# Kernel tuning notes

Measured on AMD Instinct MI355X. Metric: run time of the kernel, lower is better.

Reference implementation:

```python
import jax, jax.numpy as jnp
import numpy as np

N, E = 50000, 800000
IN, HID, OUT = 128, 32, 8


def setup_inputs() -> dict:
    key = jax.random.key(0)
    ks = jax.random.split(key, 20)
    f32 = jnp.float32
    def rn(k, shape, s=0.1):
        return (jax.random.normal(k, shape, dtype=f32) * s)
    return {
        'x': jax.random.normal(ks[0], (N, IN), dtype=f32),
        'edge_index': jax.random.randint(ks[1], (2, E), 0, N, dtype=jnp.int32),
        'edge_attr': jax.random.uniform(ks[2], (E, 1), dtype=f32),
        # layer 1: heads=4, out=HID, concat -> 4*HID channels
        'w1l': rn(ks[3], (IN, 4 * HID)), 'b1l': rn(ks[4], (4 * HID,)),
        'w1r': rn(ks[5], (IN, 4 * HID)), 'b1r': rn(ks[6], (4 * HID,)),
        'w1e': rn(ks[7], (1, 4 * HID)),
        'att1': rn(ks[8], (4, HID)), 'bias1': rn(ks[9], (4 * HID,)),
        # layer 2: heads=2, out=HID, mean over heads -> HID channels
        'w2l': rn(ks[10], (4 * HID, 2 * HID)), 'b2l': rn(ks[11], (2 * HID,)),
        'w2r': rn(ks[12], (4 * HID, 2 * HID)), 'b2r': rn(ks[13], (2 * HID,)),
        'w2e': rn(ks[14], (1, 2 * HID)),
        'att2': rn(ks[15], (2, HID)), 'bias2': rn(ks[16], (HID,)),
        'wc': rn(ks[17], (HID, OUT)), 'bc': rn(ks[18], (OUT,)),
    }


def _add_self_loops(edge_index, edge_attr, n):
    # PyG GATv2Conv adds self-loops; edge feature for loops = mean of edge_attr
    loop = jnp.arange(n, dtype=edge_index.dtype)
    src = jnp.concatenate([edge_index[0], loop])
    dst = jnp.concatenate([edge_index[1], loop])
    mean_attr = jnp.broadcast_to(edge_attr.mean(axis=0), (n, edge_attr.shape[1]))
    ea = jnp.concatenate([edge_attr, mean_attr], axis=0)
    return src, dst, ea


def _gatv2(x, src, dst, eattr, Wl, bl, Wr, br, We, att, bias, heads, out, concat):
    n = x.shape[0]
    xl = (x @ Wl + bl).reshape(n, heads, out)   # source transform (messages)
    xr = (x @ Wr + br).reshape(n, heads, out)   # target transform
    e = (eattr @ We).reshape(-1, heads, out)    # edge embedding
    z = jax.nn.leaky_relu(xl[src] + xr[dst] + e, negative_slope=0.2)  # [Etot,H,D]
    score = jnp.einsum('ehd,hd->eh', z, att)
    # segment softmax over incoming edges of each destination node
    smax = jax.ops.segment_max(score, dst, num_segments=n)
    ex = jnp.exp(score - smax[dst])
    denom = jax.ops.segment_sum(ex, dst, num_segments=n)
    alpha = ex / denom[dst]                     # [Etot,H]
    agg = jax.ops.segment_sum(xl[src] * alpha[..., None], dst, num_segments=n)
    o = agg.reshape(n, heads * out) if concat else agg.mean(axis=1)
    return o + bias


def reference(x, edge_index, edge_attr, w1l, b1l, w1r, b1r, w1e, att1, bias1,
              w2l, b2l, w2r, b2r, w2e, att2, bias2, wc, bc):
    src, dst, ea = _add_self_loops(edge_index, edge_attr, x.shape[0])
    h = _gatv2(x, src, dst, ea, w1l, b1l, w1r, b1r, w1e, att1, bias1, 4, HID, True)
    h = jax.nn.elu(h)
    # dropout p=0.4 is training-only; reference is eval mode (identity)
    h = _gatv2(h, src, dst, ea, w2l, b2l, w2r, b2r, w2e, att2, bias2, 2, HID, False)
    h = jax.nn.elu(h)
    return h @ wc + bc
```

## Files before the change

kernel.cpp:

```cpp
#include <hip/hip_runtime.h>
#include <hip/hip_fp16.h>
#include <math.h>

typedef _Float16 h2_t __attribute__((ext_vector_type(2)));
typedef _Float16 h4_t __attribute__((ext_vector_type(4)));
typedef _Float16 h8_t __attribute__((ext_vector_type(8)));
typedef float f4_t __attribute__((ext_vector_type(4)));
typedef float f8_t __attribute__((ext_vector_type(8)));

#define PRE_BLOCKS 512
#define SB 512
#define NBUK_PAD 800

__device__ inline h8_t load8f_to_h8(const float* p) {
    float4 a = *(const float4*)p;
    float4 b = *(const float4*)(p + 4);
    h8_t r;
    r[0] = (_Float16)a.x; r[1] = (_Float16)a.y; r[2] = (_Float16)a.z; r[3] = (_Float16)a.w;
    r[4] = (_Float16)b.x; r[5] = (_Float16)b.y; r[6] = (_Float16)b.z; r[7] = (_Float16)b.w;
    return r;
}

__device__ inline h4_t load4f_to_h4(const float* p) {
    float4 a = *(const float4*)p;
    h4_t r;
    r[0] = (_Float16)a.x; r[1] = (_Float16)a.y; r[2] = (_Float16)a.z; r[3] = (_Float16)a.w;
    return r;
}

__device__ inline float dot8h(h8_t a, h8_t b, float s) {
    s = __builtin_amdgcn_fdot2(__builtin_shufflevector(a, a, 0, 1),
                               __builtin_shufflevector(b, b, 0, 1), s, false);
    s = __builtin_amdgcn_fdot2(__builtin_shufflevector(a, a, 2, 3),
                               __builtin_shufflevector(b, b, 2, 3), s, false);
    s = __builtin_amdgcn_fdot2(__builtin_shufflevector(a, a, 4, 5),
                               __builtin_shufflevector(b, b, 4, 5), s, false);
    s = __builtin_amdgcn_fdot2(__builtin_shufflevector(a, a, 6, 7),
                               __builtin_shufflevector(b, b, 6, 7), s, false);
    return s;
}

__device__ inline float dot4h(h4_t a, h4_t b, float s) {
    s = __builtin_amdgcn_fdot2(__builtin_shufflevector(a, a, 0, 1),
                               __builtin_shufflevector(b, b, 0, 1), s, false);
    s = __builtin_amdgcn_fdot2(__builtin_shufflevector(a, a, 2, 3),
                               __builtin_shufflevector(b, b, 2, 3), s, false);
    return s;
}

__device__ inline float elu1(float v) { return v > 0.f ? v : __expf(v) - 1.f; }

struct MA {
    const float* x;
    const float* eattr;
    const int* ei;
    const float *w1l, *b1l, *w1r, *b1r, *w1e, *att1, *bias1;
    const float *w2l, *b2l, *w2r, *b2r, *w2e, *att2, *bias2;
    const float *wc, *bc;
    float* out;
    _Float16 *xh, *xl1h, *xr1h, *h1h, *xl2h, *xr2h;
    _Float16 *p1l, *p1r, *p2l, *p2r;
    int *deg, *offb;
    unsigned* parth;
    unsigned *tstart, *tot;
    unsigned* smeanq;
    unsigned long long* tmp;
    unsigned* flags;
    float* part;
    unsigned* edges;
    int N, E, NW, NBK, CE;
    float invE;
};


__device__ inline void phase_packw(const MA& a, int g) {
    const float* W;
    _Float16* P;
    int M, lg;
    if (g < 2048)      { W = a.w1l; P = a.p1l; M = 128; lg = g; }
    else if (g < 4096) { W = a.w1r; P = a.p1r; M = 128; lg = g - 2048; }
    else if (g < 5120) { W = a.w2l; P = a.p2l; M = 64;  lg = g - 4096; }
    else               { W = a.w2r; P = a.p2r; M = 64;  lg = g - 5120; }
    int ln = lg & 63;
    int s = (lg >> 6) & 3;
    int tt = lg >> 8;
    int m = ln & 15, quad = ln >> 4;
    h8_t v;
#pragma unroll
    for (int j = 0; j < 8; ++j)
        v[j] = (_Float16)W[(size_t)(s * 32 + quad * 8 + j) * M + tt * 16 + m];
    *(h8_t*)(P + (size_t)lg * 8) = v;
}

template <int NT>
__device__ inline void phase_mm_tile(const MA& a, const _Float16* X, int rt, int lane,
                                     const _Float16* Pl, const float* bl, _Float16* Yl,
                                     const _Float16* Pr, const float* br, _Float16* Yr) {
    int nrow = lane & 15, quad = lane >> 4;
    int row = rt * 16 + nrow;
    if (row >= a.N) return;
    const _Float16* xp = X + (size_t)row * 128 + quad * 8;
    h8_t bf0 = *(const h8_t*)(xp);
    h8_t bf1 = *(const h8_t*)(xp + 32);
    h8_t bf2 = *(const h8_t*)(xp + 64);
    h8_t bf3 = *(const h8_t*)(xp + 96);
#pragma unroll
    for (int w = 0; w < 2; ++w) {
        const _Float16* P = w ? Pr : Pl;
        const float* bias = w ? br : bl;
        _Float16* Y = w ? Yr : Yl;
#pragma unroll
        for (int t2 = 0; t2 < NT; ++t2) {
            f4_t acc = {0.f, 0.f, 0.f, 0.f};
            const _Float16* pb = P + (size_t)t2 * 2048 + (size_t)lane * 8;
            acc = __builtin_amdgcn_mfma_f32_16x16x32_f16(*(const h8_t*)pb, bf0, acc, 0, 0, 0);
            acc = __builtin_amdgcn_mfma_f32_16x16x32_f16(*(const h8_t*)(pb + 512), bf1, acc, 0, 0, 0);
            acc = __builtin_amdgcn_mfma_f32_16x16x32_f16(*(const h8_t*)(pb + 1024), bf2, acc, 0, 0, 0);
            acc = __builtin_amdgcn_mfma_f32_16x16x32_f16(*(const h8_t*)(pb + 1536), bf3, acc, 0, 0, 0);
            float4 bv = *(const float4*)(bias + t2 * 16 + quad * 4);
            h4_t o;
            o[0] = (_Float16)(acc[0] + bv.x);
            o[1] = (_Float16)(acc[1] + bv.y);
            o[2] = (_Float16)(acc[2] + bv.z);
            o[3] = (_Float16)(acc[3] + bv.w);
            *(h4_t*)(Y + (size_t)row * (NT * 16) + t2 * 16 + quad * 4) = o;
        }
    }
}


__global__ __launch_bounds__(256) void k_pre(MA a) {
    if (blockIdx.x >= PRE_BLOCKS) {
        int g = (blockIdx.x - PRE_BLOCKS) * 256 + threadIdx.x;
        if (g < 6144) phase_packw(a, g);
        return;
    }
    __shared__ unsigned bh[NBUK_PAD];
    __shared__ float sd[4];
    int tx = threadIdx.x;
    for (int j = tx; j < NBUK_PAD; j += 256) bh[j] = 0u;

    int t = blockIdx.x * 256 + tx;
    const int stride = PRE_BLOCKS * 256;
    for (int i = t; i < NBUK_PAD; i += stride) a.flags[i] = 0u;
    int nchunk = (a.N * 128) >> 3;
    for (int i = t; i < nchunk; i += stride) {
        h8_t v = load8f_to_h8(a.x + (size_t)i * 8);
        *(h8_t*)(a.xh + (size_t)i * 8) = v;
    }
    float s = 0.f;
    for (int i = t; i < a.E; i += stride) s += a.eattr[i];
    for (int o = 1; o < 64; o <<= 1) s += __shfl_xor(s, o, 64);
    if ((tx & 63) == 0) sd[tx >> 6] = s;
    __syncthreads();
    if (tx == 0) a.part[blockIdx.x] = sd[0] + sd[1] + sd[2] + sd[3];

    int e0 = blockIdx.x * a.CE, e1 = min(e0 + a.CE, a.E);
    for (int e = e0 + tx; e < e1; e += 256)
        atomicAdd(&bh[((unsigned)a.ei[a.E + e]) >> 6], 1u);
    __syncthreads();
    for (int j = tx; j < NBUK_PAD; j += 256)
        a.parth[(size_t)blockIdx.x * NBUK_PAD + j] = bh[j];
}


__global__ __launch_bounds__(512, 1) void k_colscan(MA a) {
    __shared__ unsigned lds[512];
    __shared__ unsigned sbase;
    __shared__ float sd[8];
    int tx = threadIdx.x;
    int b = blockIdx.x;
    unsigned v = a.parth[(size_t)tx * NBUK_PAD + b];
    lds[tx] = v;
    __syncthreads();
    for (int o = 1; o < 512; o <<= 1) {
        unsigned u = (tx >= o) ? lds[tx - o] : 0u;
        __syncthreads();
        lds[tx] += u;
        __syncthreads();
    }
    unsigned T = lds[511];
    unsigned excl = lds[tx] - v;
    if (tx == 0) {
        unsigned run = 0;
        if (b == 0) {
            atomicExch(&a.flags[0], (2u << 30) | T);
        } else {
            atomicExch(&a.flags[b], (1u << 30) | T);
            int j = b - 1;
            while (true) {
                unsigned f = atomicAdd(&a.flags[j], 0u);
                unsigned st = f >> 30;
                if (st == 0u) continue;
                run += f & 0x3FFFFFFFu;
                if (st == 2u) break;
                --j;
            }
            atomicExch(&a.flags[b], (2u << 30) | (run + T));
        }
        a.tstart[b] = run;
        a.tot[b] = T;
        sbase = run;
    }
    __syncthreads();
    a.parth[(size_t)tx * NBUK_PAD + b] = sbase + excl;

    if (b == 0) {
        float s = a.part[tx];
        for (int o = 1; o < 64; o <<= 1) s += __shfl_xor(s, o, 64);
        if ((tx & 63) == 0) sd[tx >> 6] = s;
        __syncthreads();
        if (tx == 0) {
            float m = 0.f;
#pragma unroll
            for (int k = 0; k < 8; ++k) m += sd[k];
            a.smeanq[0] = (unsigned)__float2int_rn(m * a.invE * 255.f);
        }
    }
}


__global__ __launch_bounds__(256) void k_scatter(MA a) {
    int bid = blockIdx.x;
    if (bid < a.NW) {
        int wid = bid * 4 + (threadIdx.x >> 6);
        int ntile = (a.N + 15) / 16;
        if (wid < ntile)
            phase_mm_tile<8>(a, a.xh, wid, threadIdx.x & 63,
                             a.p1l, a.b1l, a.xl1h, a.p1r, a.b1r, a.xr1h);
        return;
    }
    __shared__ unsigned cur[NBUK_PAD];
    int s = bid - a.NW;
    int tx = threadIdx.x;
    for (int j = tx; j < NBUK_PAD; j += 256)
        cur[j] = a.parth[(size_t)s * NBUK_PAD + j];
    __syncthreads();
    int e0 = s * a.CE, e1 = min(e0 + a.CE, a.E);
    for (int e = e0 + tx; e < e1; e += 256) {
        int d = a.ei[a.E + e];
        unsigned src = (unsigned)a.ei[e];
        unsigned q = (unsigned)__float2int_rn(a.eattr[e] * 255.f);
        unsigned pos = atomicAdd(&cur[d >> 6], 1u);
        a.tmp[pos] = ((unsigned long long)(unsigned)(d & 63) << 32) |
                     (unsigned long long)(src | (q << 24));
    }
}


__global__ __launch_bounds__(256) void k_fine(MA a) {
    __shared__ int hist[64];
    __shared__ unsigned cur[64];
    __shared__ unsigned sm;
    int b = blockIdx.x;
    int tx = threadIdx.x;
    int n0 = b << 6;
    int nn = min(64, a.N - n0);
    unsigned ts = a.tstart[b], T = a.tot[b];
    if (tx < 64) hist[tx] = 0;
    if (tx == 0) sm = a.smeanq[0];
    __syncthreads();
    for (unsigned i = tx; i < T; i += 256) {
        unsigned long long v = a.tmp[ts + i];
        atomicAdd(&hist[(int)((v >> 32) & 63)], 1);
    }
    __syncthreads();
    if (tx < 64) {
        int deg1 = hist[tx] + 1;
        int vsc = deg1;
#pragma unroll
        for (int o = 1; o < 64; o <<= 1) {
            int u = __shfl_up(vsc, o, 64);
            if (tx >= o) vsc += u;
        }
        int off = (int)ts + n0 + (vsc - deg1);
        if (tx < nn) {
            a.offb[n0 + tx] = off;
            a.deg[n0 + tx] = deg1;
            a.edges[off] = (unsigned)(n0 + tx) | (sm << 24);
        }
        cur[tx] = (unsigned)(off + 1);
    }
    __syncthreads();
    for (unsigned i = tx; i < T; i += 256) {
        unsigned long long v = a.tmp[ts + i];
        int loc = (int)((v >> 32) & 63);
        unsigned pos = atomicAdd(&cur[loc], 1u);
        a.edges[pos] = (unsigned)v;
    }
}


__global__ __launch_bounds__(256) void k_node1(MA a) {
    int lane = threadIdx.x & 63;
    int node = blockIdx.x * 4 + (threadIdx.x >> 6);
    if (node >= a.N) return;
    int g = lane >> 4;
    int q = lane & 15;
    int c0 = q * 8;

    h8_t xrv = *(const h8_t*)(a.xr1h + (size_t)node * 128 + c0);
    h8_t wev = load8f_to_h8(a.w1e + c0);
    h8_t atv = load8f_to_h8(a.att1 + c0);
    int start = a.offb[node];
    int deg1 = a.deg[node];
    int last = deg1 - 1;

    float l = 0.f;
    f8_t acc = {0.f, 0.f, 0.f, 0.f, 0.f, 0.f, 0.f, 0.f};
    for (int i = 0; i < deg1; i += 16) {
        int s0 = i + g, s1 = i + 4 + g, s2 = i + 8 + g, s3 = i + 12 + g;
        unsigned p0 = a.edges[start + min(s0, last)];
        unsigned p1 = a.edges[start + min(s1, last)];
        unsigned p2 = a.edges[start + min(s2, last)];
        unsigned p3 = a.edges[start + min(s3, last)];
        h8_t x0 = *(const h8_t*)(a.xl1h + (size_t)(p0 & 0x00FFFFFFu) * 128 + c0);
        h8_t x1 = *(const h8_t*)(a.xl1h + (size_t)(p1 & 0x00FFFFFFu) * 128 + c0);
        h8_t x2 = *(const h8_t*)(a.xl1h + (size_t)(p2 & 0x00FFFFFFu) * 128 + c0);
        h8_t x3 = *(const h8_t*)(a.xl1h + (size_t)(p3 & 0x00FFFFFFu) * 128 + c0);
        float e0 = (float)(p0 >> 24) * (1.f / 255.f);
        float e1 = (float)(p1 >> 24) * (1.f / 255.f);
        float e2 = (float)(p2 >> 24) * (1.f / 255.f);
        float e3 = (float)(p3 >> 24) * (1.f / 255.f);
        h8_t z0 = x0 + xrv + wev * (_Float16)e0;
        z0 = __builtin_elementwise_max(z0, z0 * (_Float16)0.2f);
        float sc0 = dot8h(z0, atv, 0.f);
        h8_t z1 = x1 + xrv + wev * (_Float16)e1;
        z1 = __builtin_elementwise_max(z1, z1 * (_Float16)0.2f);
        float sc1 = dot8h(z1, atv, 0.f);
        h8_t z2 = x2 + xrv + wev * (_Float16)e2;
        z2 = __builtin_elementwise_max(z2, z2 * (_Float16)0.2f);
        float sc2 = dot8h(z2, atv, 0.f);
        h8_t z3 = x3 + xrv + wev * (_Float16)e3;
        z3 = __builtin_elementwise_max(z3, z3 * (_Float16)0.2f);
        float sc3 = dot8h(z3, atv, 0.f);
        sc0 += __shfl_xor(sc0, 1, 64); sc0 += __shfl_xor(sc0, 2, 64);
        sc1 += __shfl_xor(sc1, 1, 64); sc1 += __shfl_xor(sc1, 2, 64);
        sc2 += __shfl_xor(sc2, 1, 64); sc2 += __shfl_xor(sc2, 2, 64);
        sc3 += __shfl_xor(sc3, 1, 64); sc3 += __shfl_xor(sc3, 2, 64);
        float pA = (s0 < deg1) ? __expf(fminf(sc0, 60.f)) : 0.f;
        float pB = (s1 < deg1) ? __expf(fminf(sc1, 60.f)) : 0.f;
        float pC = (s2 < deg1) ? __expf(fminf(sc2, 60.f)) : 0.f;
        float pD = (s3 < deg1) ? __expf(fminf(sc3, 60.f)) : 0.f;
        l += (pA + pB) + (pC + pD);
#pragma unroll
        for (int k = 0; k < 8; ++k)
            acc[k] = fmaf(pA, (float)x0[k],
                     fmaf(pB, (float)x1[k],
                     fmaf(pC, (float)x2[k], fmaf(pD, (float)x3[k], acc[k]))));
    }
#pragma unroll
    for (int k = 0; k < 8; ++k) {
        acc[k] += __shfl_xor(acc[k], 16, 64);
        acc[k] += __shfl_xor(acc[k], 32, 64);
    }
    l += __shfl_xor(l, 16, 64);
    l += __shfl_xor(l, 32, 64);
    if (g == 0) {
        float inv = 1.f / l;
        float4 b0 = *(const float4*)(a.bias1 + c0);
        float4 b1 = *(const float4*)(a.bias1 + c0 + 4);
        float bb[8] = {b0.x, b0.y, b0.z, b0.w, b1.x, b1.y, b1.z, b1.w};
        h8_t o;
#pragma unroll
        for (int k = 0; k < 8; ++k) o[k] = (_Float16)elu1(fmaf(acc[k], inv, bb[k]));
        *(h8_t*)(a.h1h + (size_t)node * 128 + c0) = o;
    }
}


__global__ __launch_bounds__(256) void k_mm4(MA a) {
    int wid = blockIdx.x * 4 + (threadIdx.x >> 6);
    int ntile = (a.N + 15) / 16;
    if (wid >= ntile) return;
    phase_mm_tile<4>(a, a.h1h, wid, threadIdx.x & 63,
                     a.p2l, a.b2l, a.xl2h, a.p2r, a.b2r, a.xr2h);
}


__global__ __launch_bounds__(256) void k_node2(MA a) {
    __shared__ float h2s[16][33];
    int tid = threadIdx.x;
    int lane = tid & 63;
    int wib = tid >> 6;
    int sub = lane >> 4;
    int r = lane & 15;
    int nloc = wib * 4 + sub;
    int node = blockIdx.x * 16 + nloc;
    int c0 = r * 4;

    if (node < a.N) {
        h4_t xrv = *(const h4_t*)(a.xr2h + (size_t)node * 64 + c0);
        h4_t wev = load4f_to_h4(a.w2e + c0);
        h4_t atv = load4f_to_h4(a.att2 + c0);
        int start = a.offb[node];
        int deg1 = a.deg[node];
        int last = deg1 - 1;
        float l = 0.f;
        float acc[4] = {0.f, 0.f, 0.f, 0.f};
        for (int i = 0; i < deg1; i += 4) {
            unsigned p[4];
            h4_t xv[4];
#pragma unroll
            for (int j = 0; j < 4; ++j) p[j] = a.edges[start + min(i + j, last)];
#pragma unroll
            for (int j = 0; j < 4; ++j)
                xv[j] = *(const h4_t*)(a.xl2h + (size_t)(p[j] & 0x00FFFFFFu) * 64 + c0);
#pragma unroll
            for (int j = 0; j < 4; ++j) {
                float ea = (float)(p[j] >> 24) * (1.f / 255.f);
                h4_t z = xv[j] + xrv + wev * (_Float16)ea;
                z = __builtin_elementwise_max(z, z * (_Float16)0.2f);
                float sc = dot4h(z, atv, 0.f);
                sc += __shfl_xor(sc, 1, 64);
                sc += __shfl_xor(sc, 2, 64);
                sc += __shfl_xor(sc, 4, 64);
                float pp = (i + j < deg1) ? __expf(fminf(sc, 60.f)) : 0.f;
                l += pp;
#pragma unroll
                for (int k = 0; k < 4; ++k) acc[k] = fmaf(pp, (float)xv[j][k], acc[k]);
            }
        }
        float inv = 1.f / l;
#pragma unroll
        for (int k = 0; k < 4; ++k) {
            float norm = acc[k] * inv;
            float other = __shfl_xor(norm, 8, 64);
            float v = 0.5f * (norm + other);
            if (r < 8) h2s[nloc][c0 + k] = elu1(v + a.bias2[c0 + k]);
        }
    }
    __syncthreads();
    if (tid < 128) {
        int n = tid >> 3, j = tid & 7;
        int gnode = blockIdx.x * 16 + n;
        if (gnode < a.N) {
            float acc = a.bc[j];
#pragma unroll 8
            for (int d = 0; d < 32; ++d) acc = fmaf(h2s[n][d], a.wc[d * 8 + j], acc);
            a.out[(size_t)gnode * 8 + j] = acc;
        }
    }
}


extern "C" void kernel_launch(void* const* d_in, const int* in_sizes, int n_in,
                              void* d_out, int out_size, void* d_ws, size_t ws_size,
                              hipStream_t stream) {
    const int N = in_sizes[0] / 128;
    const int E = in_sizes[2];
    const int tot = E + N;

    char* ws = (char*)d_ws;
    size_t o = 0;
    auto alloc = [&](size_t bytes) -> void* {
        void* p = ws + o;
        o += (bytes + 255) & ~(size_t)255;
        return p;
    };
    MA a;
    a.x     = (const float*)d_in[0];
    a.ei    = (const int*)d_in[1];
    a.eattr = (const float*)d_in[2];
    a.w1l = (const float*)d_in[3];  a.b1l = (const float*)d_in[4];
    a.w1r = (const float*)d_in[5];  a.b1r = (const float*)d_in[6];
    a.w1e = (const float*)d_in[7];  a.att1 = (const float*)d_in[8];
    a.bias1 = (const float*)d_in[9];
    a.w2l = (const float*)d_in[10]; a.b2l = (const float*)d_in[11];
    a.w2r = (const float*)d_in[12]; a.b2r = (const float*)d_in[13];
    a.w2e = (const float*)d_in[14]; a.att2 = (const float*)d_in[15];
    a.bias2 = (const float*)d_in[16];
    a.wc = (const float*)d_in[17];  a.bc = (const float*)d_in[18];
    a.out = (float*)d_out;

    a.xh   = (_Float16*)alloc((size_t)N * 128 * 2);
    a.xl1h = (_Float16*)alloc((size_t)N * 128 * 2);
    a.xr1h = (_Float16*)alloc((size_t)N * 128 * 2);
    a.h1h  = (_Float16*)alloc((size_t)N * 128 * 2);
    a.xl2h = (_Float16*)alloc((size_t)N * 64 * 2);
    a.xr2h = (_Float16*)alloc((size_t)N * 64 * 2);
    a.p1l  = (_Float16*)alloc(128 * 128 * 2);
    a.p1r  = (_Float16*)alloc(128 * 128 * 2);
    a.p2l  = (_Float16*)alloc(128 * 64 * 2);
    a.p2r  = (_Float16*)alloc(128 * 64 * 2);
    a.deg  = (int*)alloc((size_t)N * 4);
    a.offb = (int*)alloc((size_t)N * 4);
    a.parth  = (unsigned*)alloc((size_t)SB * NBUK_PAD * 4);
    a.tstart = (unsigned*)alloc(NBUK_PAD * 4);
    a.tot    = (unsigned*)alloc(NBUK_PAD * 4);
    a.smeanq = (unsigned*)alloc(256);
    a.flags  = (unsigned*)alloc(1024 * 4);
    a.part   = (float*)alloc(PRE_BLOCKS * 4);
    a.tmp    = (unsigned long long*)alloc((size_t)E * 8);
    a.edges  = (unsigned*)alloc((size_t)tot * 4);
    a.N = N;
    a.E = E;
    a.NW = (N + 63) / 64;
    a.NBK = (N + 63) >> 6;
    a.CE = (E + SB - 1) / SB;
    a.invE = 1.0f / (float)E;

    k_pre<<<PRE_BLOCKS + 24, 256, 0, stream>>>(a);
    k_colscan<<<a.NBK, 512, 0, stream>>>(a);
    k_scatter<<<a.NW + SB, 256, 0, stream>>>(a);
    k_fine<<<a.NBK, 256, 0, stream>>>(a);
    k_node1<<<(N + 3) / 4, 256, 0, stream>>>(a);
    k_mm4<<<(N + 63) / 64, 256, 0, stream>>>(a);
    k_node2<<<(N + 15) / 16, 256, 0, stream>>>(a);
}
```

Before: 262.0 us.

## Map one node per 16 lanes in layer-1 aggregation and simplify gather addressing

Layer-1 node aggregation now gives each 16-lane group its own destination node, four nodes per wavefront, instead of splitting one node's edges across four lane groups. This drops the cross-group shuffle reduction and the idle groups on low-degree nodes, but each group now walks all edges of its node serially, so load balance across the wavefront depends on degree variance. Gather addresses in both aggregation kernels are built with 32-bit shifts and ORs into byte offsets instead of 64-bit multiplies, trimming integer instructions.

```diff
diff --git a/kernel.cpp b/kernel.cpp
--- a/kernel.cpp
+++ b/kernel.cpp
@@ -292,32 +292,31 @@
 
 
 __global__ __launch_bounds__(256) void k_node1(MA a) {
-    int lane = threadIdx.x & 63;
-    int node = blockIdx.x * 4 + (threadIdx.x >> 6);
+    int tid = threadIdx.x;
+    int q = tid & 15;
+    int node = blockIdx.x * 16 + (tid >> 4);
     if (node >= a.N) return;
-    int g = lane >> 4;
-    int q = lane & 15;
-    int c0 = q * 8;
-
-    h8_t xrv = *(const h8_t*)(a.xr1h + (size_t)node * 128 + c0);
-    h8_t wev = load8f_to_h8(a.w1e + c0);
-    h8_t atv = load8f_to_h8(a.att1 + c0);
-    int start = a.offb[node];
+    unsigned cb = (unsigned)(q * 16);
+
+    h8_t xrv = *(const h8_t*)((const char*)a.xr1h + ((unsigned)node << 8) + cb);
+    h8_t wev = load8f_to_h8(a.w1e + q * 8);
+    h8_t atv = load8f_to_h8(a.att1 + q * 8);
+    const unsigned* ep = a.edges + a.offb[node];
     int deg1 = a.deg[node];
     int last = deg1 - 1;
+    const char* xb = (const char*)a.xl1h;
 
     float l = 0.f;
     f8_t acc = {0.f, 0.f, 0.f, 0.f, 0.f, 0.f, 0.f, 0.f};
-    for (int i = 0; i < deg1; i += 16) {
-        int s0 = i + g, s1 = i + 4 + g, s2 = i + 8 + g, s3 = i + 12 + g;
-        unsigned p0 = a.edges[start + min(s0, last)];
-        unsigned p1 = a.edges[start + min(s1, last)];
-        unsigned p2 = a.edges[start + min(s2, last)];
-        unsigned p3 = a.edges[start + min(s3, last)];
-        h8_t x0 = *(const h8_t*)(a.xl1h + (size_t)(p0 & 0x00FFFFFFu) * 128 + c0);
-        h8_t x1 = *(const h8_t*)(a.xl1h + (size_t)(p1 & 0x00FFFFFFu) * 128 + c0);
-        h8_t x2 = *(const h8_t*)(a.xl1h + (size_t)(p2 & 0x00FFFFFFu) * 128 + c0);
-        h8_t x3 = *(const h8_t*)(a.xl1h + (size_t)(p3 & 0x00FFFFFFu) * 128 + c0);
+    for (int i = 0; i < deg1; i += 4) {
+        unsigned p0 = ep[i];
+        unsigned p1 = ep[min(i + 1, last)];
+        unsigned p2 = ep[min(i + 2, last)];
+        unsigned p3 = ep[min(i + 3, last)];
+        h8_t x0 = *(const h8_t*)(xb + (((p0 & 0x00FFFFFFu) << 8) | cb));
+        h8_t x1 = *(const h8_t*)(xb + (((p1 & 0x00FFFFFFu) << 8) | cb));
+        h8_t x2 = *(const h8_t*)(xb + (((p2 & 0x00FFFFFFu) << 8) | cb));
+        h8_t x3 = *(const h8_t*)(xb + (((p3 & 0x00FFFFFFu) << 8) | cb));
         float e0 = (float)(p0 >> 24) * (1.f / 255.f);
         float e1 = (float)(p1 >> 24) * (1.f / 255.f);
         float e2 = (float)(p2 >> 24) * (1.f / 255.f);
@@ -338,10 +337,10 @@
         sc1 += __shfl_xor(sc1, 1, 64); sc1 += __shfl_xor(sc1, 2, 64);
         sc2 += __shfl_xor(sc2, 1, 64); sc2 += __shfl_xor(sc2, 2, 64);
         sc3 += __shfl_xor(sc3, 1, 64); sc3 += __shfl_xor(sc3, 2, 64);
-        float pA = (s0 < deg1) ? __expf(fminf(sc0, 60.f)) : 0.f;
-        float pB = (s1 < deg1) ? __expf(fminf(sc1, 60.f)) : 0.f;
-        float pC = (s2 < deg1) ? __expf(fminf(sc2, 60.f)) : 0.f;
-        float pD = (s3 < deg1) ? __expf(fminf(sc3, 60.f)) : 0.f;
+        float pA = __expf(fminf(sc0, 60.f));
+        float pB = (i + 1 < deg1) ? __expf(fminf(sc1, 60.f)) : 0.f;
+        float pC = (i + 2 < deg1) ? __expf(fminf(sc2, 60.f)) : 0.f;
+        float pD = (i + 3 < deg1) ? __expf(fminf(sc3, 60.f)) : 0.f;
         l += (pA + pB) + (pC + pD);
 #pragma unroll
         for (int k = 0; k < 8; ++k)
@@ -349,23 +348,14 @@
                      fmaf(pB, (float)x1[k],
                      fmaf(pC, (float)x2[k], fmaf(pD, (float)x3[k], acc[k]))));
     }
-#pragma unroll
-    for (int k = 0; k < 8; ++k) {
-        acc[k] += __shfl_xor(acc[k], 16, 64);
-        acc[k] += __shfl_xor(acc[k], 32, 64);
-    }
-    l += __shfl_xor(l, 16, 64);
-    l += __shfl_xor(l, 32, 64);
-    if (g == 0) {
-        float inv = 1.f / l;
-        float4 b0 = *(const float4*)(a.bias1 + c0);
-        float4 b1 = *(const float4*)(a.bias1 + c0 + 4);
-        float bb[8] = {b0.x, b0.y, b0.z, b0.w, b1.x, b1.y, b1.z, b1.w};
-        h8_t o;
-#pragma unroll
-        for (int k = 0; k < 8; ++k) o[k] = (_Float16)elu1(fmaf(acc[k], inv, bb[k]));
-        *(h8_t*)(a.h1h + (size_t)node * 128 + c0) = o;
-    }
+    float inv = 1.f / l;
+    float4 b0 = *(const float4*)(a.bias1 + q * 8);
+    float4 b1 = *(const float4*)(a.bias1 + q * 8 + 4);
+    float bb[8] = {b0.x, b0.y, b0.z, b0.w, b1.x, b1.y, b1.z, b1.w};
+    h8_t o;
+#pragma unroll
+    for (int k = 0; k < 8; ++k) o[k] = (_Float16)elu1(fmaf(acc[k], inv, bb[k]));
+    *(h8_t*)((char*)a.h1h + ((unsigned)node << 8) + cb) = o;
 }
 
 
@@ -393,19 +383,21 @@
         h4_t xrv = *(const h4_t*)(a.xr2h + (size_t)node * 64 + c0);
         h4_t wev = load4f_to_h4(a.w2e + c0);
         h4_t atv = load4f_to_h4(a.att2 + c0);
-        int start = a.offb[node];
+        const unsigned* ep = a.edges + a.offb[node];
         int deg1 = a.deg[node];
         int last = deg1 - 1;
+        const char* xb = (const char*)a.xl2h;
+        unsigned cb = (unsigned)(c0 * 2);
         float l = 0.f;
         float acc[4] = {0.f, 0.f, 0.f, 0.f};
         for (int i = 0; i < deg1; i += 4) {
             unsigned p[4];
             h4_t xv[4];
 #pragma unroll
-            for (int j = 0; j < 4; ++j) p[j] = a.edges[start + min(i + j, last)];
+            for (int j = 0; j < 4; ++j) p[j] = ep[min(i + j, last)];
 #pragma unroll
             for (int j = 0; j < 4; ++j)
-                xv[j] = *(const h4_t*)(a.xl2h + (size_t)(p[j] & 0x00FFFFFFu) * 64 + c0);
+                xv[j] = *(const h4_t*)(xb + (((p[j] & 0x00FFFFFFu) << 7) | cb));
 #pragma unroll
             for (int j = 0; j < 4; ++j) {
                 float ea = (float)(p[j] >> 24) * (1.f / 255.f);
@@ -504,7 +496,7 @@
     k_colscan<<<a.NBK, 512, 0, stream>>>(a);
     k_scatter<<<a.NW + SB, 256, 0, stream>>>(a);
     k_fine<<<a.NBK, 256, 0, stream>>>(a);
-    k_node1<<<(N + 3) / 4, 256, 0, stream>>>(a);
+    k_node1<<<(N + 15) / 16, 256, 0, stream>>>(a);
     k_mm4<<<(N + 63) / 64, 256, 0, stream>>>(a);
     k_node2<<<(N + 15) / 16, 256, 0, stream>>>(a);
 }
```

New measurement: 256.6 us. -2.1%, faster.
